# Kernel optimization log

Hardware: AMD Instinct MI355X
Metric: run time of the kernel (lower is better)

The kernel has to match this reference:

```python
import jax, jax.numpy as jnp
import numpy as np

N = 2048
T = 8192
OUT_DIM = 1
G, B, M = 2.0, 10.0, 1.5
DT, TAU = 0.001, 1.0


def _unit_centered(x):
    x = x - x.mean()
    return x / (jnp.linalg.norm(x) + 1e-12)


def setup_inputs() -> dict:
    key = jax.random.key(0)
    k_I, k_h0, k_W, k_u, k_v, k_rw, k_rb = jax.random.split(key, 7)
    I_t = jax.random.normal(k_I, (T, N), dtype=jnp.float32)
    h0 = 0.1 * jax.random.normal(k_h0, (N,), dtype=jnp.float32)
    W = jax.random.normal(k_W, (N, N), dtype=jnp.float32) / np.sqrt(N).astype(np.float32)
    u = _unit_centered(jax.random.normal(k_u, (N,), dtype=jnp.float32))
    v = _unit_centered(jax.random.normal(k_v, (N,), dtype=jnp.float32))
    # nn.Linear default init: U(-1/sqrt(N), 1/sqrt(N))
    lim = 1.0 / np.sqrt(N)
    ro_w = jax.random.uniform(k_rw, (OUT_DIM, N), minval=-lim, maxval=lim, dtype=jnp.float32)
    ro_b = jax.random.uniform(k_rb, (OUT_DIM,), minval=-lim, maxval=lim, dtype=jnp.float32)
    return {"I_t": I_t, "h0": h0, "W": W, "u": u, "v": v, "ro_w": ro_w, "ro_b": ro_b}


def reference(I_t, h0, W, u, v, ro_w, ro_b):
    n = W.shape[0]
    # J = g*W - (b/N) 11^T + m u v^T  (the 11^T term is a constant offset)
    J = G * W - (B / n) + M * jnp.outer(u, v)  # [N, N]
    coef = jnp.float32(DT / TAU)

    def step(h, it):
        x = jax.nn.relu(h)                      # phi(h)
        h_new = h + (-h + J @ x + it) * coef    # Euler update
        y = ro_w @ h_new + ro_b                 # readout [out_dim]
        return h_new, (y, h_new)

    _, (y_t, h_t) = jax.lax.scan(step, h0, I_t)
    return y_t, h_t  # (T, out_dim), (T, N)
```

## Files before the change

kernel.cpp:

```cpp
#include <hip/hip_runtime.h>
#include <cstdint>
#include <cstddef>


constexpr int   NN   = 2048;
constexpr int   TT   = 8192;
constexpr float COEF = 0.001f;
constexpr float G_   = 2.0f;
constexpr float BOFF = 10.0f / 2048.0f;
constexpr float M_   = 1.5f;

constexpr int NBLK = 64;
constexpr int TPB  = 512;
constexpr int WPB  = TPB / 64;

typedef float f32x4 __attribute__((ext_vector_type(4)));
typedef int   i32x4 __attribute__((ext_vector_type(4)));

__device__ __forceinline__ i32x4 bc(const f32x4 x) {
  return __builtin_bit_cast(i32x4, x);
}

__global__ void init_xbufs(float* xb) {
  const int i = blockIdx.x * blockDim.x + threadIdx.x;
  __hip_atomic_store(xb + i,      0.0f,  __ATOMIC_RELAXED, __HIP_MEMORY_SCOPE_AGENT);
  __hip_atomic_store(xb + NN + i, -1.0f, __ATOMIC_RELAXED, __HIP_MEMORY_SCOPE_AGENT);
}

__device__ __forceinline__ f32x4 poll1(const float* p) {
  f32x4 c;
  asm volatile("global_load_dwordx4 %0, %1, off sc0 sc1\n\t"
               "s_waitcnt vmcnt(0)"
               : "=&v"(c) : "v"(p) : "memory");
  return c;
}

__device__ __forceinline__ void store_wt(float* p, f32x4 v) {
  asm volatile("global_store_dwordx4 %0, %1, off sc0 sc1"
               :: "v"(p), "v"(v) : "memory");
}

template <int CTRL>
__device__ __forceinline__ float xadd_dpp(float v) {
  const int t = __builtin_amdgcn_update_dpp(0, __builtin_bit_cast(int, v),
                                            CTRL, 0xF, 0xF, false);
  return v + __builtin_bit_cast(float, t);
}
template <int PAT>
__device__ __forceinline__ float xadd_swz(float v) {
  const int t = __builtin_amdgcn_ds_swizzle(__builtin_bit_cast(int, v), PAT);
  return v + __builtin_bit_cast(float, t);
}

__global__ __launch_bounds__(TPB, 2)
void rnn_persist(const float* __restrict__ I_t,
                 const float* __restrict__ h0,
                 const float* __restrict__ W,
                 const float* __restrict__ u,
                 const float* __restrict__ v,
                 float* __restrict__ out_h,
                 float* __restrict__ xbuf)
{
  __shared__ f32x4 xs[2][NN / 4];

  const int tid = threadIdx.x;
  const int l   = tid & 63;
  const int w   = tid >> 6;
  const int gw  = blockIdx.x * WPB + w;
  const int rb  = gw * 4;
  const int cb  = l * 4;

  f32x4 J[4][8];
#pragma unroll
  for (int j = 0; j < 4; ++j) {
    const float mu = M_ * u[rb + j];
#pragma unroll
    for (int k = 0; k < 8; ++k) {
      const int c = k * 256 + cb;
      const f32x4 wv = *(const f32x4*)(W + (size_t)(rb + j) * NN + c);
      const f32x4 vv = *(const f32x4*)(v + c);
      J[j][k] = G_ * wv - BOFF + mu * vv;
    }
  }

  float h[4];
#pragma unroll
  for (int j = 0; j < 4; ++j) h[j] = h0[rb + j];

  const f32x4 zero4 = {0.f, 0.f, 0.f, 0.f};

  f32x4 iva = *(const f32x4*)(I_t + rb);
  f32x4 ivb = *(const f32x4*)(I_t + (size_t)NN + rb);

  for (int t = 0; t < TT; ++t) {
    const f32x4 icur4 = (t & 1) ? ivb : iva;
    const int bsel = t & 1;

    f32x4 c;
    if (t == 0) {
      const f32x4 hv = *(const f32x4*)(h0 + w * 256 + cb);
      c = __builtin_elementwise_max(hv, zero4);
    } else {
      const bool enc = ((t >> 1) & 1) != 0;
      const float* pb = xbuf + bsel * NN + w * 256 + cb;
      unsigned spins = 0;
      if (enc) {
        for (;;) {
          c = poll1(pb);
          const i32x4 b = bc(c);
          if (__all(((b.x & b.y) & (b.z & b.w)) < 0)) break;
          if (++spins > (1u << 22)) break;
        }
      } else {
        for (;;) {
          c = poll1(pb);
          const i32x4 b = bc(c);
          if (__all(((b.x | b.y) | (b.z | b.w)) >= 0)) break;
          if (++spins > (1u << 22)) break;
        }
      }
      i32x4 b = bc(c);
      b &= 0x7fffffff;
      c = __builtin_bit_cast(f32x4, b);
    }

    if (t + 2 < TT) {
      const f32x4 nv = *(const f32x4*)(I_t + (size_t)(t + 2) * NN + rb);
      if (t & 1) ivb = nv; else iva = nv;
    }

    xs[bsel][w * 64 + l] = c;
    __syncthreads();

    f32x4 p4[4] = {zero4, zero4, zero4, zero4};
#pragma unroll
    for (int k = 0; k < 8; ++k) {
      const f32x4 xv = xs[bsel][k * 64 + l];
#pragma unroll
      for (int j = 0; j < 4; ++j)
        p4[j] = __builtin_elementwise_fma(J[j][k], xv, p4[j]);
    }
    float p[4];
#pragma unroll
    for (int j = 0; j < 4; ++j)
      p[j] = (p4[j].x + p4[j].y) + (p4[j].z + p4[j].w);

#pragma unroll
    for (int j = 0; j < 4; ++j) {
      p[j] += __shfl_xor(p[j], 32, 64);
      p[j] = xadd_swz<0x401F>(p[j]);
      p[j] = xadd_dpp<0x128>(p[j]);
      p[j] = xadd_swz<0x101F>(p[j]);
      p[j] = xadd_dpp<0x4E>(p[j]);
      p[j] = xadd_dpp<0xB1>(p[j]);
    }

    const float ic[4] = {icur4.x, icur4.y, icur4.z, icur4.w};
#pragma unroll
    for (int j = 0; j < 4; ++j)
      h[j] = fmaf(COEF, p[j] + ic[j] - h[j], h[j]);

    if (t + 1 < TT) {
      const bool encN = (((t + 1) >> 1) & 1) != 0;
      if (l == 0) {
        i32x4 e;
        e.x = __builtin_bit_cast(int, fmaxf(h[0], 0.f));
        e.y = __builtin_bit_cast(int, fmaxf(h[1], 0.f));
        e.z = __builtin_bit_cast(int, fmaxf(h[2], 0.f));
        e.w = __builtin_bit_cast(int, fmaxf(h[3], 0.f));
        if (encN) e |= 0x80000000; else e &= 0x7fffffff;
        store_wt(xbuf + ((t + 1) & 1) * NN + rb, __builtin_bit_cast(f32x4, e));
      }
    }
    if (l == 0) {
      f32x4 hv; hv.x = h[0]; hv.y = h[1]; hv.z = h[2]; hv.w = h[3];
      *(f32x4*)(out_h + (size_t)t * NN + rb) = hv;
    }
  }
}

__global__ __launch_bounds__(256)
void readout(const float* __restrict__ h_all,
             const float* __restrict__ ro_w,
             const float* __restrict__ ro_b,
             float* __restrict__ y)
{
  __shared__ float red[4];
  const int t   = blockIdx.x;
  const int tid = threadIdx.x;
  const float* h = h_all + (size_t)t * NN;
  const int base = tid * 8;

  const float4 a0 = *(const float4*)(h + base);
  const float4 a1 = *(const float4*)(h + base + 4);
  const float4 w0 = *(const float4*)(ro_w + base);
  const float4 w1 = *(const float4*)(ro_w + base + 4);

  float s = a0.x * w0.x + a0.y * w0.y + a0.z * w0.z + a0.w * w0.w
          + a1.x * w1.x + a1.y * w1.y + a1.z * w1.z + a1.w * w1.w;
#pragma unroll
  for (int m = 32; m >= 1; m >>= 1) s += __shfl_xor(s, m, 64);

  if ((tid & 63) == 0) red[tid >> 6] = s;
  __syncthreads();
  if (tid == 0) y[t] = red[0] + red[1] + red[2] + red[3] + ro_b[0];
}

extern "C" void kernel_launch(void* const* d_in, const int* in_sizes, int n_in,
                              void* d_out, int out_size, void* d_ws, size_t ws_size,
                              hipStream_t stream)
{
  const float* I_t  = (const float*)d_in[0];
  const float* h0   = (const float*)d_in[1];
  const float* W    = (const float*)d_in[2];
  const float* u    = (const float*)d_in[3];
  const float* v    = (const float*)d_in[4];
  const float* ro_w = (const float*)d_in[5];
  const float* ro_b = (const float*)d_in[6];

  float* y    = (float*)d_out;
  float* outh = (float*)d_out + TT;

  float* xbuf = (float*)d_ws;

  init_xbufs<<<NN / TPB, TPB, 0, stream>>>(xbuf);
  rnn_persist<<<NBLK, TPB, 0, stream>>>(I_t, h0, W, u, v, outh, xbuf);
  readout<<<TT, 256, 0, stream>>>(outh, ro_w, ro_b, y);
}
```

Baseline: 16.74 ms.

## Replace block barrier with LDS flag polling and replicate exchange buffers

Drops the per-step __syncthreads. Each wave now writes its polled sign-encoded slice into LDS, then spins on LDS reads until every entry carries the expected phase sign, so waves no longer wait on a full block barrier. The global exchange buffer is replicated R times (up to 8, depending on workspace size). Lanes 0..R-1 of each wave write one copy each, so blocks poll different replicas and contention on shared cache lines drops. The cost is extra store traffic, LDS spinning, and a reliance on how the sign-encoding interacts with relaxed LDS ordering.

```diff
diff --git a/kernel.cpp b/kernel.cpp
--- a/kernel.cpp
+++ b/kernel.cpp
@@ -17,14 +17,12 @@
 typedef float f32x4 __attribute__((ext_vector_type(4)));
 typedef int   i32x4 __attribute__((ext_vector_type(4)));
 
-__device__ __forceinline__ i32x4 bc(const f32x4 x) {
-  return __builtin_bit_cast(i32x4, x);
-}
-
-__global__ void init_xbufs(float* xb) {
+__device__ __forceinline__ i32x4 bc(const f32x4 x) { return __builtin_bit_cast(i32x4, x); }
+__device__ __forceinline__ f32x4 fc(const i32x4 x) { return __builtin_bit_cast(f32x4, x); }
+
+__global__ void init_xbufs(float* xb, int total) {
   const int i = blockIdx.x * blockDim.x + threadIdx.x;
-  __hip_atomic_store(xb + i,      0.0f,  __ATOMIC_RELAXED, __HIP_MEMORY_SCOPE_AGENT);
-  __hip_atomic_store(xb + NN + i, -1.0f, __ATOMIC_RELAXED, __HIP_MEMORY_SCOPE_AGENT);
+  if (i < total) xb[i] = ((i >> 11) & 1) ? -1.0f : 0.0f;
 }
 
 __device__ __forceinline__ f32x4 poll1(const float* p) {
@@ -40,6 +38,26 @@
                :: "v"(p), "v"(v) : "memory");
 }
 
+__device__ __forceinline__ void lds_read8(unsigned addr, f32x4 x[8]) {
+  asm volatile(
+      "ds_read_b128 %0, %8 offset:0\n\t"
+      "ds_read_b128 %1, %8 offset:1024\n\t"
+      "ds_read_b128 %2, %8 offset:2048\n\t"
+      "ds_read_b128 %3, %8 offset:3072\n\t"
+      "ds_read_b128 %4, %8 offset:4096\n\t"
+      "ds_read_b128 %5, %8 offset:5120\n\t"
+      "ds_read_b128 %6, %8 offset:6144\n\t"
+      "ds_read_b128 %7, %8 offset:7168\n\t"
+      "s_waitcnt lgkmcnt(0)"
+      : "=&v"(x[0]), "=&v"(x[1]), "=&v"(x[2]), "=&v"(x[3]),
+        "=&v"(x[4]), "=&v"(x[5]), "=&v"(x[6]), "=&v"(x[7])
+      : "v"(addr)
+      : "memory");
+}
+__device__ __forceinline__ void lds_write16(unsigned addr, f32x4 v) {
+  asm volatile("ds_write_b128 %0, %1" :: "v"(addr), "v"(v) : "memory");
+}
+
 template <int CTRL>
 __device__ __forceinline__ float xadd_dpp(float v) {
   const int t = __builtin_amdgcn_update_dpp(0, __builtin_bit_cast(int, v),
@@ -52,14 +70,15 @@
   return v + __builtin_bit_cast(float, t);
 }
 
-__global__ __launch_bounds__(TPB, 2)
+__global__ __launch_bounds__(TPB, 1)
 void rnn_persist(const float* __restrict__ I_t,
                  const float* __restrict__ h0,
                  const float* __restrict__ W,
                  const float* __restrict__ u,
                  const float* __restrict__ v,
                  float* __restrict__ out_h,
-                 float* __restrict__ xbuf)
+                 float* __restrict__ xbuf,
+                 int R)
 {
   __shared__ f32x4 xs[2][NN / 4];
 
@@ -69,6 +88,7 @@
   const int gw  = blockIdx.x * WPB + w;
   const int rb  = gw * 4;
   const int cb  = l * 4;
+  const int rrep = blockIdx.x & (R - 1);
 
   f32x4 J[4][8];
 #pragma unroll
@@ -88,57 +108,83 @@
   for (int j = 0; j < 4; ++j) h[j] = h0[rb + j];
 
   const f32x4 zero4 = {0.f, 0.f, 0.f, 0.f};
+  const unsigned xs_base = (unsigned)(size_t)(&xs[0][0]);
+
+  {
+    const f32x4 m0 = {-0.0f, -0.0f, -0.0f, -0.0f};
+    xs[0][tid] = m0;
+    xs[1][tid] = m0;
+    __syncthreads();
+  }
 
   f32x4 iva = *(const f32x4*)(I_t + rb);
   f32x4 ivb = *(const f32x4*)(I_t + (size_t)NN + rb);
 
   for (int t = 0; t < TT; ++t) {
     const f32x4 icur4 = (t & 1) ? ivb : iva;
-    const int bsel = t & 1;
-
-    f32x4 c;
+    const int  bsel = t & 1;
+    const bool enc  = ((t >> 1) & 1) != 0;
+
+    f32x4 cenc;
     if (t == 0) {
       const f32x4 hv = *(const f32x4*)(h0 + w * 256 + cb);
-      c = __builtin_elementwise_max(hv, zero4);
+      i32x4 b = bc(__builtin_elementwise_max(hv, zero4));
+      b &= 0x7fffffff;
+      cenc = fc(b);
     } else {
-      const bool enc = ((t >> 1) & 1) != 0;
-      const float* pb = xbuf + bsel * NN + w * 256 + cb;
+      const float* pb = xbuf + (size_t)rrep * (2 * NN) + bsel * NN + w * 256 + cb;
       unsigned spins = 0;
       if (enc) {
         for (;;) {
-          c = poll1(pb);
-          const i32x4 b = bc(c);
+          cenc = poll1(pb);
+          const i32x4 b = bc(cenc);
           if (__all(((b.x & b.y) & (b.z & b.w)) < 0)) break;
           if (++spins > (1u << 22)) break;
         }
       } else {
         for (;;) {
-          c = poll1(pb);
-          const i32x4 b = bc(c);
+          cenc = poll1(pb);
+          const i32x4 b = bc(cenc);
           if (__all(((b.x | b.y) | (b.z | b.w)) >= 0)) break;
           if (++spins > (1u << 22)) break;
         }
       }
-      i32x4 b = bc(c);
-      b &= 0x7fffffff;
-      c = __builtin_bit_cast(f32x4, b);
-    }
+    }
+
+    lds_write16(xs_base + bsel * 8192 + w * 1024 + l * 16, cenc);
 
     if (t + 2 < TT) {
       const f32x4 nv = *(const f32x4*)(I_t + (size_t)(t + 2) * NN + rb);
       if (t & 1) ivb = nv; else iva = nv;
     }
 
-    xs[bsel][w * 64 + l] = c;
-    __syncthreads();
+    f32x4 xv[8];
+    {
+      const unsigned raddr = xs_base + bsel * 8192 + l * 16;
+      unsigned spins = 0;
+      for (;;) {
+        lds_read8(raddr, xv);
+        const i32x4 a0 = bc(xv[0]), a1 = bc(xv[1]), a2 = bc(xv[2]), a3 = bc(xv[3]);
+        const i32x4 a4 = bc(xv[4]), a5 = bc(xv[5]), a6 = bc(xv[6]), a7 = bc(xv[7]);
+        if (enc) {
+          i32x4 s = (a0 & a1) & (a2 & a3); s &= (a4 & a5) & (a6 & a7);
+          if (__all(((s.x & s.y) & (s.z & s.w)) < 0)) break;
+        } else {
+          i32x4 s = (a0 | a1) | (a2 | a3); s |= (a4 | a5) | (a6 | a7);
+          if (__all(((s.x | s.y) | (s.z | s.w)) >= 0)) break;
+        }
+        if (++spins > (1u << 20)) break;
+      }
+    }
 
     f32x4 p4[4] = {zero4, zero4, zero4, zero4};
 #pragma unroll
     for (int k = 0; k < 8; ++k) {
-      const f32x4 xv = xs[bsel][k * 64 + l];
+      i32x4 b = bc(xv[k]); b &= 0x7fffffff;
+      const f32x4 xd = fc(b);
 #pragma unroll
       for (int j = 0; j < 4; ++j)
-        p4[j] = __builtin_elementwise_fma(J[j][k], xv, p4[j]);
+        p4[j] = __builtin_elementwise_fma(J[j][k], xd, p4[j]);
     }
     float p[4];
 #pragma unroll
@@ -162,15 +208,14 @@
 
     if (t + 1 < TT) {
       const bool encN = (((t + 1) >> 1) & 1) != 0;
-      if (l == 0) {
-        i32x4 e;
-        e.x = __builtin_bit_cast(int, fmaxf(h[0], 0.f));
-        e.y = __builtin_bit_cast(int, fmaxf(h[1], 0.f));
-        e.z = __builtin_bit_cast(int, fmaxf(h[2], 0.f));
-        e.w = __builtin_bit_cast(int, fmaxf(h[3], 0.f));
-        if (encN) e |= 0x80000000; else e &= 0x7fffffff;
-        store_wt(xbuf + ((t + 1) & 1) * NN + rb, __builtin_bit_cast(f32x4, e));
-      }
+      i32x4 e;
+      e.x = __builtin_bit_cast(int, fmaxf(h[0], 0.f));
+      e.y = __builtin_bit_cast(int, fmaxf(h[1], 0.f));
+      e.z = __builtin_bit_cast(int, fmaxf(h[2], 0.f));
+      e.w = __builtin_bit_cast(int, fmaxf(h[3], 0.f));
+      if (encN) e |= 0x80000000; else e &= 0x7fffffff;
+      if (l < R)
+        store_wt(xbuf + (size_t)l * (2 * NN) + ((t + 1) & 1) * NN + rb, fc(e));
     }
     if (l == 0) {
       f32x4 hv; hv.x = h[0]; hv.y = h[1]; hv.z = h[2]; hv.w = h[3];
@@ -223,7 +268,13 @@
 
   float* xbuf = (float*)d_ws;
 
-  init_xbufs<<<NN / TPB, TPB, 0, stream>>>(xbuf);
-  rnn_persist<<<NBLK, TPB, 0, stream>>>(I_t, h0, W, u, v, outh, xbuf);
+  int R = 1;
+  if      (ws_size >= (size_t)8 * 2 * NN * 4) R = 8;
+  else if (ws_size >= (size_t)4 * 2 * NN * 4) R = 4;
+  else if (ws_size >= (size_t)2 * 2 * NN * 4) R = 2;
+
+  const int total = R * 2 * NN;
+  init_xbufs<<<(total + TPB - 1) / TPB, TPB, 0, stream>>>(xbuf, total);
+  rnn_persist<<<NBLK, TPB, 0, stream>>>(I_t, h0, W, u, v, outh, xbuf, R);
   readout<<<TT, 256, 0, stream>>>(outh, ro_w, ro_b, y);
 }
```

Result: slower. 21.30 ms (+27.3%).

## Replace per-step block barrier with sign-encoded LDS flag polling

Applied to the files above, without the earlier changes.

Removes the __syncthreads per timestep. Each wave writes its sign-encoded slice of x into LDS, and consumer waves spin on each LDS chunk until the sign bits match the current parity. This lets waves start their partial dot products as soon as individual chunks arrive, instead of waiting for the whole block. In exchange it adds LDS spin loops that serialize each read with a waitcnt. It also relies on LDS write visibility ordering without a barrier, and on double-buffer parity being enough to prevent overwrite races.

```diff
diff --git a/kernel.cpp b/kernel.cpp
--- a/kernel.cpp
+++ b/kernel.cpp
@@ -17,14 +17,13 @@
 typedef float f32x4 __attribute__((ext_vector_type(4)));
 typedef int   i32x4 __attribute__((ext_vector_type(4)));
 
-__device__ __forceinline__ i32x4 bc(const f32x4 x) {
-  return __builtin_bit_cast(i32x4, x);
-}
+__device__ __forceinline__ i32x4 bc(const f32x4 x) { return __builtin_bit_cast(i32x4, x); }
+__device__ __forceinline__ f32x4 fc(const i32x4 x) { return __builtin_bit_cast(f32x4, x); }
 
 __global__ void init_xbufs(float* xb) {
   const int i = blockIdx.x * blockDim.x + threadIdx.x;
-  __hip_atomic_store(xb + i,      0.0f,  __ATOMIC_RELAXED, __HIP_MEMORY_SCOPE_AGENT);
-  __hip_atomic_store(xb + NN + i, -1.0f, __ATOMIC_RELAXED, __HIP_MEMORY_SCOPE_AGENT);
+  xb[i]      = 0.0f;
+  xb[NN + i] = -1.0f;
 }
 
 __device__ __forceinline__ f32x4 poll1(const float* p) {
@@ -38,6 +37,17 @@
 __device__ __forceinline__ void store_wt(float* p, f32x4 v) {
   asm volatile("global_store_dwordx4 %0, %1, off sc0 sc1"
                :: "v"(p), "v"(v) : "memory");
+}
+
+__device__ __forceinline__ f32x4 lds_read1(unsigned addr) {
+  f32x4 x;
+  asm volatile("ds_read_b128 %0, %1\n\t"
+               "s_waitcnt lgkmcnt(0)"
+               : "=&v"(x) : "v"(addr) : "memory");
+  return x;
+}
+__device__ __forceinline__ void lds_write16(unsigned addr, f32x4 v) {
+  asm volatile("ds_write_b128 %0, %1" :: "v"(addr), "v"(v) : "memory");
 }
 
 template <int CTRL>
@@ -88,57 +98,74 @@
   for (int j = 0; j < 4; ++j) h[j] = h0[rb + j];
 
   const f32x4 zero4 = {0.f, 0.f, 0.f, 0.f};
+  const unsigned xs_base = (unsigned)(size_t)(&xs[0][0]);
+
+  {
+    const f32x4 m0 = {-0.0f, -0.0f, -0.0f, -0.0f};
+    xs[0][tid] = m0;
+    xs[1][tid] = m0;
+    __syncthreads();
+  }
 
   f32x4 iva = *(const f32x4*)(I_t + rb);
   f32x4 ivb = *(const f32x4*)(I_t + (size_t)NN + rb);
 
   for (int t = 0; t < TT; ++t) {
     const f32x4 icur4 = (t & 1) ? ivb : iva;
-    const int bsel = t & 1;
-
-    f32x4 c;
+    const int  bsel = t & 1;
+    const bool enc  = ((t >> 1) & 1) != 0;
+
+    f32x4 cenc;
     if (t == 0) {
       const f32x4 hv = *(const f32x4*)(h0 + w * 256 + cb);
-      c = __builtin_elementwise_max(hv, zero4);
+      i32x4 b = bc(__builtin_elementwise_max(hv, zero4));
+      b &= 0x7fffffff;
+      cenc = fc(b);
     } else {
-      const bool enc = ((t >> 1) & 1) != 0;
       const float* pb = xbuf + bsel * NN + w * 256 + cb;
       unsigned spins = 0;
       if (enc) {
         for (;;) {
-          c = poll1(pb);
-          const i32x4 b = bc(c);
+          cenc = poll1(pb);
+          const i32x4 b = bc(cenc);
           if (__all(((b.x & b.y) & (b.z & b.w)) < 0)) break;
           if (++spins > (1u << 22)) break;
         }
       } else {
         for (;;) {
-          c = poll1(pb);
-          const i32x4 b = bc(c);
+          cenc = poll1(pb);
+          const i32x4 b = bc(cenc);
           if (__all(((b.x | b.y) | (b.z | b.w)) >= 0)) break;
           if (++spins > (1u << 22)) break;
         }
       }
-      i32x4 b = bc(c);
-      b &= 0x7fffffff;
-      c = __builtin_bit_cast(f32x4, b);
-    }
+    }
+
+    lds_write16(xs_base + bsel * 8192 + w * 1024 + l * 16, cenc);
 
     if (t + 2 < TT) {
       const f32x4 nv = *(const f32x4*)(I_t + (size_t)(t + 2) * NN + rb);
       if (t & 1) ivb = nv; else iva = nv;
     }
 
-    xs[bsel][w * 64 + l] = c;
-    __syncthreads();
-
     f32x4 p4[4] = {zero4, zero4, zero4, zero4};
+    const unsigned rbase = xs_base + bsel * 8192 + l * 16;
 #pragma unroll
     for (int k = 0; k < 8; ++k) {
-      const f32x4 xv = xs[bsel][k * 64 + l];
+      f32x4 xe;
+      unsigned spins = 0;
+      for (;;) {
+        xe = lds_read1(rbase + k * 1024);
+        const i32x4 b = bc(xe);
+        if (enc) { if (__all(((b.x & b.y) & (b.z & b.w)) < 0)) break; }
+        else     { if (__all(((b.x | b.y) | (b.z | b.w)) >= 0)) break; }
+        if (++spins > (1u << 20)) break;
+      }
+      i32x4 b = bc(xe); b &= 0x7fffffff;
+      const f32x4 xd = fc(b);
 #pragma unroll
       for (int j = 0; j < 4; ++j)
-        p4[j] = __builtin_elementwise_fma(J[j][k], xv, p4[j]);
+        p4[j] = __builtin_elementwise_fma(J[j][k], xd, p4[j]);
     }
     float p[4];
 #pragma unroll
@@ -169,7 +196,7 @@
         e.z = __builtin_bit_cast(int, fmaxf(h[2], 0.f));
         e.w = __builtin_bit_cast(int, fmaxf(h[3], 0.f));
         if (encN) e |= 0x80000000; else e &= 0x7fffffff;
-        store_wt(xbuf + ((t + 1) & 1) * NN + rb, __builtin_bit_cast(f32x4, e));
+        store_wt(xbuf + ((t + 1) & 1) * NN + rb, fc(e));
       }
     }
     if (l == 0) {
```

New measurement: 24.41 ms. 45.8% more time.

## Replicate exchange buffer across R copies to spread polling contention

Applied to the files above, without the earlier changes.

Each wave now writes its relu'd hidden slice to up to R (2/4/8) replicas of the double-buffered exchange buffer, one replica per lane, and each block polls the replica selected by its block index. Fewer blocks spin on the same cache lines, which is meant to cut coherent-load contention in the per-step cross-block sync. The cost is R times more write-through stores per step and a larger workspace to initialize. R is chosen from the available workspace size.

```diff
diff --git a/kernel.cpp b/kernel.cpp
--- a/kernel.cpp
+++ b/kernel.cpp
@@ -17,14 +17,12 @@
 typedef float f32x4 __attribute__((ext_vector_type(4)));
 typedef int   i32x4 __attribute__((ext_vector_type(4)));
 
-__device__ __forceinline__ i32x4 bc(const f32x4 x) {
-  return __builtin_bit_cast(i32x4, x);
-}
-
-__global__ void init_xbufs(float* xb) {
+__device__ __forceinline__ i32x4 bc(const f32x4 x) { return __builtin_bit_cast(i32x4, x); }
+__device__ __forceinline__ f32x4 fc(const i32x4 x) { return __builtin_bit_cast(f32x4, x); }
+
+__global__ void init_xbufs(float* xb, int total) {
   const int i = blockIdx.x * blockDim.x + threadIdx.x;
-  __hip_atomic_store(xb + i,      0.0f,  __ATOMIC_RELAXED, __HIP_MEMORY_SCOPE_AGENT);
-  __hip_atomic_store(xb + NN + i, -1.0f, __ATOMIC_RELAXED, __HIP_MEMORY_SCOPE_AGENT);
+  if (i < total) xb[i] = ((i >> 11) & 1) ? -1.0f : 0.0f;
 }
 
 __device__ __forceinline__ f32x4 poll1(const float* p) {
@@ -59,7 +57,8 @@
                  const float* __restrict__ u,
                  const float* __restrict__ v,
                  float* __restrict__ out_h,
-                 float* __restrict__ xbuf)
+                 float* __restrict__ xbuf,
+                 int R)
 {
   __shared__ f32x4 xs[2][NN / 4];
 
@@ -69,6 +68,7 @@
   const int gw  = blockIdx.x * WPB + w;
   const int rb  = gw * 4;
   const int cb  = l * 4;
+  const int rrep = blockIdx.x & (R - 1);
 
   f32x4 J[4][8];
 #pragma unroll
@@ -102,7 +102,7 @@
       c = __builtin_elementwise_max(hv, zero4);
     } else {
       const bool enc = ((t >> 1) & 1) != 0;
-      const float* pb = xbuf + bsel * NN + w * 256 + cb;
+      const float* pb = xbuf + (size_t)rrep * (2 * NN) + bsel * NN + w * 256 + cb;
       unsigned spins = 0;
       if (enc) {
         for (;;) {
@@ -162,15 +162,14 @@
 
     if (t + 1 < TT) {
       const bool encN = (((t + 1) >> 1) & 1) != 0;
-      if (l == 0) {
-        i32x4 e;
-        e.x = __builtin_bit_cast(int, fmaxf(h[0], 0.f));
-        e.y = __builtin_bit_cast(int, fmaxf(h[1], 0.f));
-        e.z = __builtin_bit_cast(int, fmaxf(h[2], 0.f));
-        e.w = __builtin_bit_cast(int, fmaxf(h[3], 0.f));
-        if (encN) e |= 0x80000000; else e &= 0x7fffffff;
-        store_wt(xbuf + ((t + 1) & 1) * NN + rb, __builtin_bit_cast(f32x4, e));
-      }
+      i32x4 e;
+      e.x = __builtin_bit_cast(int, fmaxf(h[0], 0.f));
+      e.y = __builtin_bit_cast(int, fmaxf(h[1], 0.f));
+      e.z = __builtin_bit_cast(int, fmaxf(h[2], 0.f));
+      e.w = __builtin_bit_cast(int, fmaxf(h[3], 0.f));
+      if (encN) e |= 0x80000000; else e &= 0x7fffffff;
+      if (l < R)
+        store_wt(xbuf + (size_t)l * (2 * NN) + ((t + 1) & 1) * NN + rb, fc(e));
     }
     if (l == 0) {
       f32x4 hv; hv.x = h[0]; hv.y = h[1]; hv.z = h[2]; hv.w = h[3];
@@ -223,7 +222,13 @@
 
   float* xbuf = (float*)d_ws;
 
-  init_xbufs<<<NN / TPB, TPB, 0, stream>>>(xbuf);
-  rnn_persist<<<NBLK, TPB, 0, stream>>>(I_t, h0, W, u, v, outh, xbuf);
+  int R = 1;
+  if      (ws_size >= (size_t)8 * 2 * NN * 4) R = 8;
+  else if (ws_size >= (size_t)4 * 2 * NN * 4) R = 4;
+  else if (ws_size >= (size_t)2 * 2 * NN * 4) R = 2;
+
+  const int total = R * 2 * NN;
+  init_xbufs<<<(total + TPB - 1) / TPB, TPB, 0, stream>>>(xbuf, total);
+  rnn_persist<<<NBLK, TPB, 0, stream>>>(I_t, h0, W, u, v, outh, xbuf, R);
   readout<<<TT, 256, 0, stream>>>(outh, ro_w, ro_b, y);
 }
```

Measured after the change: 19.80 ms. +18.3%, slower.
